# Performance work log

Measured on AMD Instinct MI355X. Metric: run time of the kernel, lower is better.

## Reference

```python
import jax, jax.numpy as jnp
import numpy as np

DIM = 512
HEADS = 8
B, H, W = 8, 32, 32
SMOOTH = 1e-4
BN_EPS = 1e-5


def _conv(x, w, pad):
    return jax.lax.conv_general_dilated(
        x, w, window_strides=(1, 1), padding=[(pad, pad), (pad, pad)],
        dimension_numbers=('NCHW', 'OIHW', 'NCHW'))


def setup_inputs() -> dict:
    key = jax.random.key(0)
    k1, k2, k3 = jax.random.split(key, 3)
    x = jax.random.normal(k1, (B, DIM, H, W), dtype=jnp.float32)
    # conv weights with fan-in style scaling for stable magnitudes
    W_qkv = jax.random.normal(k2, (3 * DIM, DIM, 3, 3), dtype=jnp.float32) * (1.0 / np.sqrt(DIM * 9))
    W_out = jax.random.normal(k3, (DIM, DIM, 1, 1), dtype=jnp.float32) * (1.0 / np.sqrt(DIM))
    gamma = jnp.ones((DIM,), dtype=jnp.float32)
    beta = jnp.zeros((DIM,), dtype=jnp.float32)
    return {"x": x, "W_qkv": W_qkv, "W_out": W_out, "gamma": gamma, "beta": beta}


def reference(x, W_qkv, W_out, gamma, beta):
    b, c, h, w = x.shape
    g = HEADS
    d = c // g
    n = h * w
    qkv = _conv(x, W_qkv, pad=1)                      # [b, 3c, h, w]
    q, k, v = jnp.split(qkv, 3, axis=1)
    # 'b (g d) h w -> b g (h w) d'
    to_seq = lambda t: t.reshape(b, g, d, n).transpose(0, 1, 3, 2)
    q, k, v = to_seq(q), to_seq(k), to_seq(v)         # [b, g, n, d]
    attn = jnp.einsum('bgid,bgjd->bgij', q, k)        # [b, g, n, n]
    qn = jnp.sqrt(jnp.sum(q * q, axis=-1) + SMOOTH)   # [b, g, n]
    kn = jnp.sqrt(jnp.sum(k * k, axis=-1) + SMOOTH)   # [b, g, n]
    attn = attn / (qn[:, :, :, None] * kn[:, :, None, :] + SMOOTH)
    out = jnp.einsum('bgij,bgjd->bgid', attn, v)      # [b, g, n, d]
    # 'b g (h w) d -> b (g d) h w'
    out = out.transpose(0, 1, 3, 2).reshape(b, c, h, w)
    out = _conv(out, W_out, pad=0)
    # BatchNorm2d (training mode: batch statistics, biased variance)
    mean = jnp.mean(out, axis=(0, 2, 3))
    var = jnp.var(out, axis=(0, 2, 3))
    out = (out - mean[None, :, None, None]) * jax.lax.rsqrt(var + BN_EPS)[None, :, None, None]
    out = out * gamma[None, :, None, None] + beta[None, :, None, None]
    return jax.nn.relu(out)
```

## Files before the change

### kernel.cpp

```cpp
#include <hip/hip_runtime.h>
#include <math.h>


#define SMOOTH 1e-4f
#define BN_EPS 1e-5f

typedef __attribute__((ext_vector_type(8))) short bf16x8;
typedef __attribute__((ext_vector_type(4))) float f32x4;
typedef __attribute__((ext_vector_type(4))) unsigned int u32x4;
typedef __attribute__((ext_vector_type(4))) unsigned short u16x4;

__device__ inline unsigned short bf16rne(float f) {
  unsigned int u = __float_as_uint(f);
  u += 0x7fff + ((u >> 16) & 1);
  return (unsigned short)(u >> 16);
}
__device__ inline float b2f(unsigned short u) {
  return __uint_as_float((unsigned int)u << 16);
}
__device__ inline float fastrcp(float x) {
#if __has_builtin(__builtin_amdgcn_rcpf)
  return __builtin_amdgcn_rcpf(x);
#else
  return 1.0f / x;
#endif
}

__global__ void repack_w(const float* __restrict__ wq,
                         unsigned short* __restrict__ wqr) {
  __shared__ float Ws[2304];
  const int tid = threadIdx.x;
  const size_t pair0 = (size_t)blockIdx.x * 256;
  for (int off = tid; off < 576; off += 256)
    *(float4*)(Ws + off * 4) = *(const float4*)(wq + pair0 * 9 + off * 4);
  __syncthreads();
#pragma unroll
  for (int t = 0; t < 9; ++t)
    wqr[(size_t)t * 786432 + pair0 + tid] = bf16rne(Ws[tid * 9 + t]);
}

__global__ void repack_x(const float* __restrict__ x,
                         unsigned short* __restrict__ xr) {
  __shared__ float Xs[64 * 132];
  const int tid = threadIdx.x;
  const int p0 = (blockIdx.x & 7) * 128;
  const int ci0 = ((blockIdx.x >> 3) & 7) * 64;
  const int b = blockIdx.x >> 6;
  for (int k = 0; k < 8; ++k) {
    int idx = tid + k * 256;
    int c4 = idx & 31, row = idx >> 5;
    *(float4*)(Xs + row * 132 + c4 * 4) =
        *(const float4*)(x + ((size_t)(b * 512 + ci0 + row)) * 1024 + p0 + c4 * 4);
  }
  __syncthreads();
  const int pl = tid >> 1, half = tid & 1;
#pragma unroll
  for (int v = 0; v < 8; ++v) {
    u16x4 pk;
#pragma unroll
    for (int e = 0; e < 4; ++e)
      pk[e] = bf16rne(Xs[(half * 32 + v * 4 + e) * 132 + pl]);
    *(u16x4*)(xr + ((size_t)(b * 1024) + p0 + pl) * 512 + ci0 + half * 32 + v * 4) = pk;
  }
}

__global__ void repack_wo(const float* __restrict__ wo,
                          unsigned short* __restrict__ wor) {
  int idx = blockIdx.x * 256 + threadIdx.x;
  wor[idx] = bf16rne(wo[idx]);
}

__global__ __launch_bounds__(256) void conv3x3_mfma(
    const unsigned short* __restrict__ wqr,
    const unsigned short* __restrict__ xr,
    unsigned short* __restrict__ qt, unsigned short* __restrict__ kt,
    unsigned short* __restrict__ vt, float* __restrict__ qn,
    float* __restrict__ kn) {
  __shared__ __align__(16) unsigned short Wl[9 * 64 * 32];
  __shared__ __align__(16) unsigned short Xl[6 * 34 * 32];
  __shared__ float Snl[128];

  const int tid = threadIdx.x;
  const int lane = tid & 63;
  const int wave = tid >> 6;
  const int wco = (wave & 1) * 32;
  const int wn = (wave >> 1) * 64;
  const int l15 = lane & 15;
  const int quad = lane >> 4;
  const int k8 = quad * 8;
  const int h0 = blockIdx.x * 4;
  const int co0 = blockIdx.y * 64;
  const int b = blockIdx.z;

  f32x4 acc[2][4];
  for (int ma = 0; ma < 2; ++ma)
    for (int nb = 0; nb < 4; ++nb) acc[ma][nb] = (f32x4){0.f, 0.f, 0.f, 0.f};

  for (int ci0 = 0; ci0 < 512; ci0 += 32) {
    __syncthreads();
    for (int idx = tid; idx < 2304; idx += 256) {
      int c4 = idx & 3;
      int co = (idx >> 2) & 63;
      int t = idx >> 8;
      *(u32x4*)(Wl + (t * 64 + co) * 32 + c4 * 8) =
          *(const u32x4*)(wqr + ((size_t)(t * 1536 + co0 + co) * 512 + ci0 + c4 * 8));
    }
    for (int idx = tid; idx < 816; idx += 256) {
      int c4 = idx & 3;
      int r = idx >> 2;
      int wi = r % 34;
      int hh = r / 34;
      int h = h0 - 1 + hh;
      int w = wi - 1;
      u32x4 v = {0u, 0u, 0u, 0u};
      if ((unsigned)h < 32u && (unsigned)w < 32u)
        v = *(const u32x4*)(xr + ((size_t)((b * 32 + h) * 32 + w) * 512 + ci0 + c4 * 8));
      *(u32x4*)(Xl + (hh * 34 + wi) * 32 + c4 * 8) = v;
    }
    __syncthreads();

#pragma unroll
    for (int t = 0; t < 9; ++t) {
      const int ky = t / 3, kx = t - ky * 3;
      bf16x8 af[2], bfr[4];
#pragma unroll
      for (int ma = 0; ma < 2; ++ma)
        af[ma] = *(const bf16x8*)(Wl + (t * 64 + wco + ma * 16 + l15) * 32 + k8);
#pragma unroll
      for (int nb = 0; nb < 4; ++nb) {
        int n = wn + nb * 16 + l15;
        int hh = (n >> 5) + ky;
        int wi = (n & 31) + kx;
        bfr[nb] = *(const bf16x8*)(Xl + (hh * 34 + wi) * 32 + k8);
      }
#pragma unroll
      for (int ma = 0; ma < 2; ++ma)
#pragma unroll
        for (int nb = 0; nb < 4; ++nb)
          acc[ma][nb] = __builtin_amdgcn_mfma_f32_16x16x32_bf16(
              af[ma], bfr[nb], acc[ma][nb], 0, 0, 0);
    }
  }

  const int sec = co0 >> 9;
  const int g = (co0 & 511) >> 6;
  const int bg = b * 8 + g;
  if (sec < 2) {
    unsigned short* dst = (sec == 0) ? qt : kt;
#pragma unroll
    for (int ma = 0; ma < 2; ++ma)
#pragma unroll
      for (int nb = 0; nb < 4; ++nb) {
        int n = wn + nb * 16 + l15;
        int p = (h0 + (n >> 5)) * 32 + (n & 31);
        int db = wco + ma * 16 + quad * 4;
        u16x4 pk;
#pragma unroll
        for (int r = 0; r < 4; ++r) pk[r] = bf16rne(acc[ma][nb][r]);
        *(u16x4*)(dst + ((size_t)bg * 1024 + p) * 64 + db) = pk;
      }
    float ps[4];
#pragma unroll
    for (int nb = 0; nb < 4; ++nb) {
      float s = 0.f;
#pragma unroll
      for (int ma = 0; ma < 2; ++ma)
#pragma unroll
        for (int r = 0; r < 4; ++r) s = fmaf(acc[ma][nb][r], acc[ma][nb][r], s);
      s += __shfl_down(s, 32);
      s += __shfl_down(s, 16);
      ps[nb] = s;
    }
    if (wco == 0 && quad == 0)
#pragma unroll
      for (int nb = 0; nb < 4; ++nb) Snl[wn + nb * 16 + l15] = ps[nb];
    __syncthreads();
    if (wco == 32 && quad == 0) {
      float* ndst = (sec == 0) ? qn : kn;
#pragma unroll
      for (int nb = 0; nb < 4; ++nb) {
        int n = wn + nb * 16 + l15;
        int p = (h0 + (n >> 5)) * 32 + (n & 31);
        ndst[bg * 1024 + p] = sqrtf(Snl[n] + ps[nb] + SMOOTH);
      }
    }
  } else {
#pragma unroll
    for (int ma = 0; ma < 2; ++ma)
#pragma unroll
      for (int nb = 0; nb < 4; ++nb) {
        int n = wn + nb * 16 + l15;
        int p = (h0 + (n >> 5)) * 32 + (n & 31);
#pragma unroll
        for (int r = 0; r < 4; ++r) {
          int d = wco + ma * 16 + quad * 4 + r;
          vt[((size_t)bg * 64 + d) * 1024 + p] = bf16rne(acc[ma][nb][r]);
        }
      }
  }
}

__global__ __launch_bounds__(256) void attn_mfma(
    const unsigned short* __restrict__ qt, const unsigned short* __restrict__ kt,
    const unsigned short* __restrict__ vt, const float* __restrict__ qn,
    const float* __restrict__ kn, unsigned short* __restrict__ aob) {
  __shared__ __align__(16) unsigned short Kl[64 * 72];
  __shared__ __align__(16) unsigned short Vl[64 * 72];
  __shared__ __align__(16) unsigned short Sl[64 * 72];

  const int tid = threadIdx.x;
  const int lane = tid & 63, wave = tid >> 6;
  const int l15 = lane & 15, quad = lane >> 4;
  const int bg = blockIdx.x;
  const int i0 = blockIdx.y * 64;
  const int iw = i0 + wave * 16;
  const int b = bg >> 3, g = bg & 7;

  bf16x8 qf[2];
#pragma unroll
  for (int ks = 0; ks < 2; ++ks)
    qf[ks] = *(const bf16x8*)(
        qt + ((size_t)bg * 1024 + iw + l15) * 64 + ks * 32 + quad * 8);

  float qn_i[4];
#pragma unroll
  for (int r = 0; r < 4; ++r) qn_i[r] = qn[bg * 1024 + iw + quad * 4 + r];

  f32x4 oacc[4];
  for (int nf = 0; nf < 4; ++nf) oacc[nf] = (f32x4){0.f, 0.f, 0.f, 0.f};

  unsigned short* Sw = Sl + wave * 16 * 72;

  for (int jt = 0; jt < 16; ++jt) {
    const int j0 = jt * 64;
    __syncthreads();
    for (int idx = tid; idx < 512; idx += 256) {
      int c8 = idx & 7, row = idx >> 3;
      *(u32x4*)(Kl + row * 72 + c8 * 8) =
          *(const u32x4*)(kt + ((size_t)bg * 1024 + j0 + row) * 64 + c8 * 8);
      *(u32x4*)(Vl + row * 72 + c8 * 8) =
          *(const u32x4*)(vt + ((size_t)bg * 64 + row) * 1024 + j0 + c8 * 8);
    }
    __syncthreads();

    f32x4 sacc[4];
    for (int nb = 0; nb < 4; ++nb) sacc[nb] = (f32x4){0.f, 0.f, 0.f, 0.f};
#pragma unroll
    for (int ks = 0; ks < 2; ++ks) {
#pragma unroll
      for (int nb = 0; nb < 4; ++nb) {
        bf16x8 kf = *(const bf16x8*)(Kl + (l15 + 16 * nb) * 72 + ks * 32 + quad * 8);
        sacc[nb] = __builtin_amdgcn_mfma_f32_16x16x32_bf16(
            qf[ks], kf, sacc[nb], 0, 0, 0);
      }
    }

#pragma unroll
    for (int nb = 0; nb < 4; ++nb) {
      float kn_j = kn[bg * 1024 + j0 + l15 + 16 * nb];
#pragma unroll
      for (int r = 0; r < 4; ++r) {
        float s = sacc[nb][r] * fastrcp(fmaf(qn_i[r], kn_j, SMOOTH));
        Sw[(quad * 4 + r) * 72 + l15 + 16 * nb] = bf16rne(s);
      }
    }
#pragma unroll
    for (int ks2 = 0; ks2 < 2; ++ks2) {
      bf16x8 sa = *(const bf16x8*)(Sw + l15 * 72 + ks2 * 32 + quad * 8);
#pragma unroll
      for (int nf = 0; nf < 4; ++nf) {
        bf16x8 vb = *(const bf16x8*)(Vl + (l15 + 16 * nf) * 72 + ks2 * 32 + quad * 8);
        oacc[nf] = __builtin_amdgcn_mfma_f32_16x16x32_bf16(sa, vb, oacc[nf], 0, 0, 0);
      }
    }
  }

#pragma unroll
  for (int nf = 0; nf < 4; ++nf)
#pragma unroll
    for (int r = 0; r < 4; ++r) {
      int i = iw + quad * 4 + r;
      int d = l15 + 16 * nf;
      aob[((size_t)(b * 1024) + i) * 512 + g * 64 + d] = bf16rne(oacc[nf][r]);
    }
}

__global__ void zero_stats(float* __restrict__ sums, float* __restrict__ sumsq) {
  int t = blockIdx.x * 256 + threadIdx.x;
  if (t < 512) {
    sums[t] = 0.f;
    sumsq[t] = 0.f;
  }
}

__global__ __launch_bounds__(256) void conv1x1_mfma(
    const unsigned short* __restrict__ wor, const unsigned short* __restrict__ aob,
    float* __restrict__ y, float* __restrict__ sums, float* __restrict__ sumsq) {
  __shared__ __align__(16) unsigned short Wl[64 * 40];
  __shared__ __align__(16) unsigned short Bl[64 * 40];

  const int tid = threadIdx.x;
  const int lane = tid & 63, wave = tid >> 6;
  const int l15 = lane & 15, quad = lane >> 4;
  const int wco = (wave & 1) * 32;
  const int wp = (wave >> 1) * 32;
  const int p0 = blockIdx.x * 64;
  const int co0 = blockIdx.y * 64;
  const int b = blockIdx.z;

  f32x4 acc[2][2];
  for (int ma = 0; ma < 2; ++ma)
    for (int nb = 0; nb < 2; ++nb) acc[ma][nb] = (f32x4){0.f, 0.f, 0.f, 0.f};

  for (int ci0 = 0; ci0 < 512; ci0 += 32) {
    __syncthreads();
    {
      int c4 = tid & 3, co = tid >> 2;
      *(u32x4*)(Wl + co * 40 + c4 * 8) =
          *(const u32x4*)(wor + (size_t)(co0 + co) * 512 + ci0 + c4 * 8);
      *(u32x4*)(Bl + co * 40 + c4 * 8) =
          *(const u32x4*)(aob + ((size_t)(b * 1024) + p0 + co) * 512 + ci0 + c4 * 8);
    }
    __syncthreads();

    bf16x8 af[2], bf[2];
#pragma unroll
    for (int ma = 0; ma < 2; ++ma)
      af[ma] = *(const bf16x8*)(Wl + (wco + ma * 16 + l15) * 40 + quad * 8);
#pragma unroll
    for (int nb = 0; nb < 2; ++nb)
      bf[nb] = *(const bf16x8*)(Bl + (wp + nb * 16 + l15) * 40 + quad * 8);
#pragma unroll
    for (int ma = 0; ma < 2; ++ma)
#pragma unroll
      for (int nb = 0; nb < 2; ++nb)
        acc[ma][nb] = __builtin_amdgcn_mfma_f32_16x16x32_bf16(
            af[ma], bf[nb], acc[ma][nb], 0, 0, 0);
  }

#pragma unroll
  for (int ma = 0; ma < 2; ++ma)
#pragma unroll
    for (int r = 0; r < 4; ++r) {
      int co = co0 + wco + ma * 16 + quad * 4 + r;
      float s1 = 0.f, s2 = 0.f;
#pragma unroll
      for (int nb = 0; nb < 2; ++nb) {
        float v = acc[ma][nb][r];
        y[((size_t)(b * 512) + co) * 1024 + p0 + wp + nb * 16 + l15] = v;
        s1 += v;
        s2 = fmaf(v, v, s2);
      }
      for (int off = 8; off >= 1; off >>= 1) {
        s1 += __shfl_down(s1, off, 16);
        s2 += __shfl_down(s2, off, 16);
      }
      if (l15 == 0) {
        atomicAdd(&sums[co], s1);
        atomicAdd(&sumsq[co], s2);
      }
    }
}

__global__ void bn_kernel(const float* __restrict__ y,
                          const float* __restrict__ sums,
                          const float* __restrict__ sumsq,
                          const float* __restrict__ gamma,
                          const float* __restrict__ beta,
                          float* __restrict__ out) {
  int idx = blockIdx.x * 256 + threadIdx.x;
  int c = (idx >> 8) & 511;
  float4 v = ((const float4*)y)[idx];
  float mean = sums[c] * (1.f / 8192.f);
  float var = sumsq[c] * (1.f / 8192.f) - mean * mean;
  float sc = gamma[c] * rsqrtf(var + BN_EPS);
  float sh = beta[c] - mean * sc;
  float4 r;
  r.x = fmaxf(0.f, fmaf(v.x, sc, sh));
  r.y = fmaxf(0.f, fmaf(v.y, sc, sh));
  r.z = fmaxf(0.f, fmaf(v.z, sc, sh));
  r.w = fmaxf(0.f, fmaf(v.w, sc, sh));
  ((float4*)out)[idx] = r;
}

extern "C" void kernel_launch(void* const* d_in, const int* in_sizes, int n_in,
                              void* d_out, int out_size, void* d_ws,
                              size_t ws_size, hipStream_t stream) {
  const float* x = (const float*)d_in[0];
  const float* wq = (const float*)d_in[1];
  const float* wo = (const float*)d_in[2];
  const float* gamma = (const float*)d_in[3];
  const float* beta = (const float*)d_in[4];
  float* out = (float*)d_out;

  unsigned short* qt = (unsigned short*)d_ws;
  unsigned short* kt = qt + (size_t)4194304;
  unsigned short* vt = kt + (size_t)4194304;
  unsigned short* aob = vt + (size_t)4194304;
  unsigned short* wqr = aob + (size_t)4194304;
  unsigned short* wor = wqr + (size_t)7077888;
  unsigned short* xr = wor + (size_t)262144;
  float* qn = (float*)(xr + (size_t)4194304);
  float* kn = qn + 65536;
  float* y = kn + 65536;
  float* sums = y + (size_t)4194304;
  float* sumsq = sums + 512;

  repack_w<<<dim3(3072), 256, 0, stream>>>(wq, wqr);
  repack_x<<<dim3(512), 256, 0, stream>>>(x, xr);
  repack_wo<<<dim3(1024), 256, 0, stream>>>(wo, wor);
  zero_stats<<<dim3(2), 256, 0, stream>>>(sums, sumsq);
  conv3x3_mfma<<<dim3(8, 24, 8), 256, 0, stream>>>(wqr, xr, qt, kt, vt, qn, kn);
  attn_mfma<<<dim3(64, 16), 256, 0, stream>>>(qt, kt, vt, qn, kn, aob);
  conv1x1_mfma<<<dim3(16, 8, 8), 256, 0, stream>>>(wor, aob, y, sums, sumsq);
  bn_kernel<<<dim3(4096), 256, 0, stream>>>(y, sums, sumsq, gamma, beta, out);
}
```

Before: 332.7 us.

## Pad input buffer and load conv3x3 tiles with async global-to-LDS copies

The repacked input is now written into a zero-padded 34x34 spatial buffer, cleared by a memset, so the conv3x3 tile loads need no bounds checks. Weight and input tiles are copied straight from global memory into LDS with global_load_lds, using a channel-chunk-major LDS layout that the MFMA operand reads index accordingly. This removes the register round trip and branching in the staging loops. The stats-zeroing kernel is folded into repack_wo to save a launch, at the cost of an extra memset over the padded buffer.

```diff
diff --git a/kernel.cpp b/kernel.cpp
--- a/kernel.cpp
+++ b/kernel.cpp
@@ -14,9 +14,6 @@
   unsigned int u = __float_as_uint(f);
   u += 0x7fff + ((u >> 16) & 1);
   return (unsigned short)(u >> 16);
-}
-__device__ inline float b2f(unsigned short u) {
-  return __uint_as_float((unsigned int)u << 16);
 }
 __device__ inline float fastrcp(float x) {
 #if __has_builtin(__builtin_amdgcn_rcpf)
@@ -24,6 +21,12 @@
 #else
   return 1.0f / x;
 #endif
+}
+
+typedef __attribute__((address_space(1))) void gvoid;
+typedef __attribute__((address_space(3))) void lvoid;
+__device__ __forceinline__ void async16(const void* g, void* l) {
+  __builtin_amdgcn_global_load_lds((gvoid*)g, (lvoid*)l, 16, 0, 0);
 }
 
 __global__ void repack_w(const float* __restrict__ wq,
@@ -40,7 +43,7 @@
 }
 
 __global__ void repack_x(const float* __restrict__ x,
-                         unsigned short* __restrict__ xr) {
+                         unsigned short* __restrict__ xrp) {
   __shared__ float Xs[64 * 132];
   const int tid = threadIdx.x;
   const int p0 = (blockIdx.x & 7) * 128;
@@ -54,30 +57,39 @@
   }
   __syncthreads();
   const int pl = tid >> 1, half = tid & 1;
+  const int p = p0 + pl;
+  const int h = p >> 5, w = p & 31;
+  unsigned short* dst =
+      xrp + ((size_t)((b * 34 + h + 1) * 34 + w + 1)) * 512 + ci0 + half * 32;
 #pragma unroll
   for (int v = 0; v < 8; ++v) {
     u16x4 pk;
 #pragma unroll
     for (int e = 0; e < 4; ++e)
       pk[e] = bf16rne(Xs[(half * 32 + v * 4 + e) * 132 + pl]);
-    *(u16x4*)(xr + ((size_t)(b * 1024) + p0 + pl) * 512 + ci0 + half * 32 + v * 4) = pk;
+    *(u16x4*)(dst + v * 4) = pk;
   }
 }
 
 __global__ void repack_wo(const float* __restrict__ wo,
-                          unsigned short* __restrict__ wor) {
+                          unsigned short* __restrict__ wor,
+                          float* __restrict__ sums, float* __restrict__ sumsq) {
   int idx = blockIdx.x * 256 + threadIdx.x;
   wor[idx] = bf16rne(wo[idx]);
+  if (blockIdx.x < 2) {
+    sums[idx] = 0.f;
+    sumsq[idx] = 0.f;
+  }
 }
 
 __global__ __launch_bounds__(256) void conv3x3_mfma(
     const unsigned short* __restrict__ wqr,
-    const unsigned short* __restrict__ xr,
+    const unsigned short* __restrict__ xrp,
     unsigned short* __restrict__ qt, unsigned short* __restrict__ kt,
     unsigned short* __restrict__ vt, float* __restrict__ qn,
     float* __restrict__ kn) {
-  __shared__ __align__(16) unsigned short Wl[9 * 64 * 32];
-  __shared__ __align__(16) unsigned short Xl[6 * 34 * 32];
+  __shared__ __align__(16) unsigned short Wl[2304 * 8];
+  __shared__ __align__(16) unsigned short Xl[816 * 8];
   __shared__ float Snl[128];
 
   const int tid = threadIdx.x;
@@ -87,7 +99,6 @@
   const int wn = (wave >> 1) * 64;
   const int l15 = lane & 15;
   const int quad = lane >> 4;
-  const int k8 = quad * 8;
   const int h0 = blockIdx.x * 4;
   const int co0 = blockIdx.y * 64;
   const int b = blockIdx.z;
@@ -98,24 +109,30 @@
 
   for (int ci0 = 0; ci0 < 512; ci0 += 32) {
     __syncthreads();
-    for (int idx = tid; idx < 2304; idx += 256) {
-      int c4 = idx & 3;
-      int co = (idx >> 2) & 63;
-      int t = idx >> 8;
-      *(u32x4*)(Wl + (t * 64 + co) * 32 + c4 * 8) =
-          *(const u32x4*)(wqr + ((size_t)(t * 1536 + co0 + co) * 512 + ci0 + c4 * 8));
-    }
-    for (int idx = tid; idx < 816; idx += 256) {
-      int c4 = idx & 3;
-      int r = idx >> 2;
-      int wi = r % 34;
-      int hh = r / 34;
-      int h = h0 - 1 + hh;
-      int w = wi - 1;
-      u32x4 v = {0u, 0u, 0u, 0u};
-      if ((unsigned)h < 32u && (unsigned)w < 32u)
-        v = *(const u32x4*)(xr + ((size_t)((b * 32 + h) * 32 + w) * 512 + ci0 + c4 * 8));
-      *(u32x4*)(Xl + (hh * 34 + wi) * 32 + c4 * 8) = v;
+#pragma unroll
+    for (int j = 0; j < 9; ++j) {
+      int c = wave + 4 * j;
+      int c4 = c / 9;
+      int t = c - c4 * 9;
+      async16(wqr + ((size_t)(t * 1536 + co0) + lane) * 512 + ci0 + c4 * 8,
+              Wl + (size_t)c * 512);
+    }
+#pragma unroll
+    for (int j = 0; j < 3; ++j) {
+      int c = wave + 4 * j;
+      int g = c * 64 + lane;
+      int c4 = g / 204;
+      int rem = g - c4 * 204;
+      int hh = rem / 34, wi = rem - hh * 34;
+      async16(xrp + ((size_t)((b * 34 + h0 + hh) * 34 + wi)) * 512 + ci0 + c4 * 8,
+              Xl + (size_t)c * 512);
+    }
+    if (wave == 0 && lane < 48) {
+      int g = 768 + lane;
+      int rem = g - 612;
+      int hh = rem / 34, wi = rem - hh * 34;
+      async16(xrp + ((size_t)((b * 34 + h0 + hh) * 34 + wi)) * 512 + ci0 + 24,
+              Xl + (size_t)768 * 8);
     }
     __syncthreads();
 
@@ -125,13 +142,14 @@
       bf16x8 af[2], bfr[4];
 #pragma unroll
       for (int ma = 0; ma < 2; ++ma)
-        af[ma] = *(const bf16x8*)(Wl + (t * 64 + wco + ma * 16 + l15) * 32 + k8);
+        af[ma] = *(const bf16x8*)(
+            Wl + ((size_t)(quad * 576 + t * 64 + wco + ma * 16 + l15)) * 8);
 #pragma unroll
       for (int nb = 0; nb < 4; ++nb) {
         int n = wn + nb * 16 + l15;
         int hh = (n >> 5) + ky;
         int wi = (n & 31) + kx;
-        bfr[nb] = *(const bf16x8*)(Xl + (hh * 34 + wi) * 32 + k8);
+        bfr[nb] = *(const bf16x8*)(Xl + ((size_t)(quad * 204 + hh * 34 + wi)) * 8);
       }
 #pragma unroll
       for (int ma = 0; ma < 2; ++ma)
@@ -283,14 +301,6 @@
       int d = l15 + 16 * nf;
       aob[((size_t)(b * 1024) + i) * 512 + g * 64 + d] = bf16rne(oacc[nf][r]);
     }
-}
-
-__global__ void zero_stats(float* __restrict__ sums, float* __restrict__ sumsq) {
-  int t = blockIdx.x * 256 + threadIdx.x;
-  if (t < 512) {
-    sums[t] = 0.f;
-    sumsq[t] = 0.f;
-  }
 }
 
 __global__ __launch_bounds__(256) void conv1x1_mfma(
@@ -399,18 +409,18 @@
   unsigned short* aob = vt + (size_t)4194304;
   unsigned short* wqr = aob + (size_t)4194304;
   unsigned short* wor = wqr + (size_t)7077888;
-  unsigned short* xr = wor + (size_t)262144;
-  float* qn = (float*)(xr + (size_t)4194304);
+  unsigned short* xrp = wor + (size_t)262144;
+  float* qn = (float*)(xrp + (size_t)4734976);
   float* kn = qn + 65536;
   float* y = kn + 65536;
   float* sums = y + (size_t)4194304;
   float* sumsq = sums + 512;
 
+  hipMemsetAsync(xrp, 0, (size_t)4734976 * 2, stream);
   repack_w<<<dim3(3072), 256, 0, stream>>>(wq, wqr);
-  repack_x<<<dim3(512), 256, 0, stream>>>(x, xr);
-  repack_wo<<<dim3(1024), 256, 0, stream>>>(wo, wor);
-  zero_stats<<<dim3(2), 256, 0, stream>>>(sums, sumsq);
-  conv3x3_mfma<<<dim3(8, 24, 8), 256, 0, stream>>>(wqr, xr, qt, kt, vt, qn, kn);
+  repack_x<<<dim3(512), 256, 0, stream>>>(x, xrp);
+  repack_wo<<<dim3(1024), 256, 0, stream>>>(wo, wor, sums, sumsq);
+  conv3x3_mfma<<<dim3(8, 24, 8), 256, 0, stream>>>(wqr, xrp, qt, kt, vt, qn, kn);
   attn_mfma<<<dim3(64, 16), 256, 0, stream>>>(qt, kt, vt, qn, kn, aob);
   conv1x1_mfma<<<dim3(16, 8, 8), 256, 0, stream>>>(wor, aob, y, sums, sumsq);
   bn_kernel<<<dim3(4096), 256, 0, stream>>>(y, sums, sumsq, gamma, beta, out);
```

After: 478.8 us. 43.9% more time.
